# Kernel optimization log

Measured on AMD Instinct MI355X. Metric: run time of the kernel, lower is better.

The kernel has to match this reference:

```python
import jax, jax.numpy as jnp
import numpy as np

N_NODES = 100000
N_EDGES = 1600000
IN_DIM = 256
HID = 128
R = 3  # num_relations


def layer_norm(h, gamma, beta, eps=1e-5):
    mu = h.mean(axis=-1, keepdims=True)
    var = ((h - mu) ** 2).mean(axis=-1, keepdims=True)
    return (h - mu) * jax.lax.rsqrt(var + eps) * gamma + beta


def rgcn_conv(h, src, dst, etype, W, root, bias):
    """PyG RGCNConv with aggr='mean'. W:[R,in,out], root:[in,out], bias:[out]."""
    N = h.shape[0]
    out_dim = W.shape[-1]
    trans = jnp.einsum('ni,rio->rno', h, W)            # [R, N, out]
    msgs = trans[etype, src]                            # [E, out] gather per edge
    seg = dst * R + etype                               # combined (node, relation) segment id
    sums = jax.ops.segment_sum(msgs, seg, num_segments=N * R)          # [N*R, out]
    cnt = jax.ops.segment_sum(jnp.ones_like(msgs[:, 0]), seg, num_segments=N * R)
    agg = (sums / jnp.maximum(cnt, 1.0)[:, None]).reshape(N, R, out_dim).sum(axis=1)
    return agg + h @ root + bias


def setup_inputs() -> dict:
    key = jax.random.key(0)
    ks = jax.random.split(key, 10)
    s = lambda *sh: 1.0 / np.sqrt(sh[-2])
    inp = {
        'x': jax.random.normal(ks[0], (N_NODES, IN_DIM), dtype=jnp.float32),
        'edge_index': jax.random.randint(ks[1], (2, N_EDGES), 0, N_NODES, dtype=jnp.int64),
        'edge_type': jax.random.randint(ks[2], (N_EDGES,), 0, R, dtype=jnp.int64),
        # layer 0: in=256 -> out=128
        'W0': jax.random.normal(ks[3], (R, IN_DIM, HID), dtype=jnp.float32) / np.sqrt(IN_DIM),
        'root0': jax.random.normal(ks[4], (IN_DIM, HID), dtype=jnp.float32) / np.sqrt(IN_DIM),
        'b0': jnp.zeros((HID,), dtype=jnp.float32),
        'g0': jnp.ones((HID,), dtype=jnp.float32),
        'be0': jnp.zeros((HID,), dtype=jnp.float32),
        # layer 1: in=128 -> out=128
        'W1': jax.random.normal(ks[5], (R, HID, HID), dtype=jnp.float32) / np.sqrt(HID),
        'root1': jax.random.normal(ks[6], (HID, HID), dtype=jnp.float32) / np.sqrt(HID),
        'b1': jnp.zeros((HID,), dtype=jnp.float32),
        'g1': jnp.ones((HID,), dtype=jnp.float32),
        'be1': jnp.zeros((HID,), dtype=jnp.float32),
        # output LayerNorm (projection is Identity since hidden==output)
        'gout': jnp.ones((HID,), dtype=jnp.float32),
        'bout': jnp.zeros((HID,), dtype=jnp.float32),
    }
    return inp


def reference(x, edge_index, edge_type, W0, root0, b0, g0, be0,
              W1, root1, b1, g1, be1, gout, bout):
    src, dst = edge_index[0], edge_index[1]
    h = rgcn_conv(x, src, dst, edge_type, W0, root0, b0)
    h = layer_norm(h, g0, be0)
    h = jax.nn.leaky_relu(h, negative_slope=0.2)  # dropout = identity (eval)
    h = rgcn_conv(h, src, dst, edge_type, W1, root1, b1)
    h = layer_norm(h, g1, be1)
    h = layer_norm(h, gout, bout)  # output_projection is Identity
    return h
```

## Files before the change

### kernel.cpp

```cpp
#include <hip/hip_runtime.h>

#define NN 100000
#define EE 1600000

#define FB2  1568
#define NR   12500
#define GBX  782
#define GB0  (GBX * 4)
#define PB0  512
#define PB1  256
#define CVB  2048

typedef unsigned short ushortT;
typedef unsigned int uintT;
typedef __attribute__((ext_vector_type(4))) float f32x4;
typedef __attribute__((ext_vector_type(8))) short bf16x8;

__device__ inline float bf2f(ushortT b) {
    return __uint_as_float(((uintT)b) << 16);
}
__device__ inline ushortT f2bf(float f) {
    uintT u = __float_as_uint(f);
    u += 0x7FFFu + ((u >> 16) & 1u);
    return (ushortT)(u >> 16);
}

__device__ inline void gload_lds16(const void* g, void* l) {
    __builtin_amdgcn_global_load_lds((const __attribute__((address_space(1))) void*)g,
                                     (__attribute__((address_space(3))) void*)l, 16, 0, 0);
}

__device__ void cvt_role(int bid, const float* __restrict__ x, ushortT* __restrict__ xb) {
    const int total = NN * 256 / 4;
    for (int i = bid * 256 + threadIdx.x; i < total; i += CVB * 256) {
        float4 v = ((const float4*)x)[i];
        ushort4 o;
        o.x = f2bf(v.x); o.y = f2bf(v.y); o.z = f2bf(v.z); o.w = f2bf(v.w);
        ((ushort4*)xb)[i] = o;
    }
}

template <int K>
__device__ void bpack_role(int bid, const float* __restrict__ W,
                           const float* __restrict__ root, ushortT* __restrict__ Bpack) {
    constexpr int KB = K / 32;
    int idx = bid * 256 + threadIdx.x;
    if (idx >= 512 * K) return;
    int j = idx & 7;
    int l = (idx >> 3) & 63;
    int blk = idx >> 9;
    int kb = blk % KB, nblk = blk / KB;
    int k = kb * 32 + (l >> 4) * 8 + j;
    int m = nblk * 16 + (l & 15);
    float v;
    if (m < 384) {
        v = W[(((size_t)(m >> 7)) * K + k) * 128 + (m & 127)];
    } else {
        v = root[(size_t)k * 128 + (m - 384)];
    }
    Bpack[idx] = f2bf(v);
}

__global__ __launch_bounds__(256) void fill_kernel(const int* __restrict__ esrc,
                                                   const int* __restrict__ edst,
                                                   const int* __restrict__ etyp,
                                                   uintT* __restrict__ cursor,
                                                   uintT* __restrict__ elist) {
    const int bid = blockIdx.x;
    const int g = bid & 7;
    const int j = bid >> 3;
    const int lo = g * NR, hi = lo + NR;
    const int base = j * 8192;
    for (int k0 = 0; k0 < 8192; k0 += 1024) {
        int e0 = base + k0 + threadIdx.x;
        int d[4];
#pragma unroll
        for (int t = 0; t < 4; ++t) {
            int e = e0 + t * 256;
            d[t] = (e < EE) ? __builtin_nontemporal_load(&edst[e]) : -1;
        }
#pragma unroll
        for (int t = 0; t < 4; ++t) {
            if (d[t] >= lo && d[t] < hi) {
                int e = e0 + t * 256;
                int s = __builtin_nontemporal_load(&esrc[e]);
                int r = __builtin_nontemporal_load(&etyp[e]);
                if ((unsigned)s < NN && (unsigned)r < 3u) {
                    uintT add = 1u + (r == 1 ? (1u << 10) : 0u) + (r == 2 ? (1u << 20) : 0u);
                    uintT old = atomicAdd(&cursor[d[t]], add);
                    uintT pos = old & 1023u;
                    if (pos < 64u) elist[(size_t)d[t] * 64 + pos] = ((uintT)s << 2) | (uintT)r;
                }
            }
        }
    }
}

__device__ inline int swz_off(int r, int g) {
    return r * 32 + ((g ^ ((r >> 1) & 3)) << 3);
}

template <int K>
__device__ void gemm_role(int bx, int by, const ushortT* __restrict__ A,
                          const ushortT* __restrict__ Bpack, ushortT* __restrict__ C,
                          int N, ushortT* As ) {
    constexpr int KB = K / 32;
    const int tid = threadIdx.x;
    const int lane = tid & 63;
    const int wid = tid >> 6;
    const int wr = wid >> 1, wc = wid & 1;
    const int bm = bx * 128;
    const int bnblk = by * 8;

    size_t src_off[2];
#pragma unroll
    for (int t = 0; t < 2; ++t) {
        int U = (wid * 2 + t) * 64 + lane;
        int r = U >> 2;
        int g = (U & 3) ^ ((r >> 1) & 3);
        int row = bm + r;
        if (row > N - 1) row = N - 1;
        src_off[t] = (size_t)row * K + g * 8;
    }

    auto stage_issue = [&](int kblk, int buf) {
#pragma unroll
        for (int t = 0; t < 2; ++t)
            gload_lds16(&A[src_off[t] + kblk * 32], &As[buf * 4096 + (wid * 2 + t) * 512]);
    };
    f32x4 acc[4][4] = {};
    bf16x8 breg[4], bnext[4];
    auto load_b = [&](int kblk, bf16x8* out) {
#pragma unroll
        for (int nb = 0; nb < 4; ++nb) {
            int nblk = bnblk + wc * 4 + nb;
            out[nb] = *(const bf16x8*)&Bpack[((size_t)(nblk * KB + kblk) * 64 + lane) * 8];
        }
    };

    stage_issue(0, 0);
    load_b(0, breg);

    for (int kblk = 0; kblk < KB; ++kblk) {
        const int cur = kblk & 1;
        __syncthreads();
        if (kblk + 1 < KB) stage_issue(kblk + 1, cur ^ 1);
        bf16x8 afrag[4];
#pragma unroll
        for (int mb = 0; mb < 4; ++mb) {
            int fr = wr * 64 + mb * 16 + (lane & 15);
            afrag[mb] = *(const bf16x8*)&As[cur * 4096 + swz_off(fr, lane >> 4)];
        }
        if (kblk + 1 < KB) load_b(kblk + 1, bnext);
#pragma unroll
        for (int mb = 0; mb < 4; ++mb)
#pragma unroll
            for (int nb = 0; nb < 4; ++nb)
                acc[mb][nb] = __builtin_amdgcn_mfma_f32_16x16x32_bf16(
                    afrag[mb], breg[nb], acc[mb][nb], 0, 0, 0);
        if (kblk + 1 < KB) {
#pragma unroll
            for (int nb = 0; nb < 4; ++nb) breg[nb] = bnext[nb];
        }
    }

#pragma unroll
    for (int mb = 0; mb < 4; ++mb) {
        int row0 = bm + wr * 64 + mb * 16 + ((lane >> 4) << 2);
#pragma unroll
        for (int nb = 0; nb < 4; ++nb) {
            int col = (bnblk + wc * 4 + nb) * 16 + (lane & 15);
#pragma unroll
            for (int q = 0; q < 4; ++q) {
                int row = row0 + q;
                if (row < N) C[(size_t)row * 512 + col] = f2bf(acc[mb][nb][q]);
            }
        }
    }
}

__global__ __launch_bounds__(256) void k1_kernel(const float* __restrict__ x,
                                                 ushortT* __restrict__ xb,
                                                 const float* __restrict__ W0,
                                                 const float* __restrict__ root0,
                                                 ushortT* __restrict__ Bpack0,
                                                 const float* __restrict__ W1,
                                                 const float* __restrict__ root1,
                                                 ushortT* __restrict__ Bpack1) {
    int bid = blockIdx.x;
    if (bid < CVB) { cvt_role(bid, x, xb); return; }
    bid -= CVB;
    if (bid < PB0) { bpack_role<256>(bid, W0, root0, Bpack0); return; }
    bid -= PB0;
    bpack_role<128>(bid, W1, root1, Bpack1);
}

__global__ __launch_bounds__(256) void gemm0_kernel(const ushortT* __restrict__ A,
                                                    const ushortT* __restrict__ Bpack,
                                                    ushortT* __restrict__ C) {
    __shared__ ushortT As[2 * 4096];
    gemm_role<256>(blockIdx.x % GBX, blockIdx.x / GBX, A, Bpack, C, NN, As);
}

__global__ __launch_bounds__(256) void gemm1_kernel(const ushortT* __restrict__ A,
                                                    const ushortT* __restrict__ Bpack,
                                                    ushortT* __restrict__ C) {
    __shared__ ushortT As[2 * 4096];
    gemm_role<128>(blockIdx.x % GBX, blockIdx.x / GBX, A, Bpack, C, NN, As);
}

template <int LAYER>
__global__ __launch_bounds__(256) void agg_finalize_kernel(
    const ushortT* __restrict__ trans, const uintT* __restrict__ elist,
    const uintT* __restrict__ cursor,
    const float* __restrict__ bias, const float* __restrict__ gamma,
    const float* __restrict__ beta, const float* __restrict__ gout,
    const float* __restrict__ bout, void* __restrict__ outp) {
    const int wid = threadIdx.x >> 6;
    const int lane = threadIdx.x & 63;
    const int n = blockIdx.x * 4 + wid;
    const int c2 = lane * 2;
    const int cbyte = c2 * 2;

    const uintT cw = cursor[n];
    int deg = (int)(cw & 1023u);
    const int cr1 = (int)((cw >> 10) & 1023u);
    const int cr2 = (int)((cw >> 20) & 1023u);
    const int cr0 = deg - cr1 - cr2;
    const float i0 = 1.0f / fmaxf((float)cr0, 1.0f);
    const float i1 = 1.0f / fmaxf((float)cr1, 1.0f);
    const float i2 = 1.0f / fmaxf((float)cr2, 1.0f);
    if (deg > 64) deg = 64;
    const char* tb = (const char*)trans;

    uintT ev_all = 0;
    if (deg > 0) ev_all = elist[(size_t)n * 64 + (lane < deg ? lane : deg - 1)];

    float p0 = 0.f, p1 = 0.f, q0 = 0.f, q1 = 0.f;
    float r0a = 0.f, r1a = 0.f, s0a = 0.f, s1a = 0.f;

    for (int i = 0; i < deg; i += 8) {
#pragma unroll
        for (int k = 0; k < 8; ++k) {
            int sl = i + k;
            int slc = sl < deg ? sl : deg - 1;
            uintT ev = (uintT)__builtin_amdgcn_readlane((int)ev_all, slc);
            uintT off = (ev >> 2) * 1024u + (ev & 3u) * 256u;
            ushort2 u = *(const ushort2*)(tb + off + cbyte);
            int r = (int)(ev & 3u);
            float wr_ = r == 0 ? i0 : (r == 1 ? i1 : i2);
            float w = sl < deg ? wr_ : 0.f;
            float f0 = w * bf2f(u.x), f1 = w * bf2f(u.y);
            if ((k & 3) == 0) { p0 += f0; p1 += f1; }
            else if ((k & 3) == 1) { q0 += f0; q1 += f1; }
            else if ((k & 3) == 2) { r0a += f0; r1a += f1; }
            else { s0a += f0; s1a += f1; }
        }
    }
    float a0 = (p0 + q0) + (r0a + s0a);
    float a1 = (p1 + q1) + (r1a + s1a);

    ushort2 rt = *(const ushort2*)&trans[(size_t)n * 512 + 384 + c2];
    float v0 = a0 + bf2f(rt.x) + bias[c2 + 0];
    float v1 = a1 + bf2f(rt.y) + bias[c2 + 1];

    float s = v0 + v1, s2 = v0 * v0 + v1 * v1;
#pragma unroll
    for (int m = 32; m >= 1; m >>= 1) {
        s += __shfl_xor(s, m);
        s2 += __shfl_xor(s2, m);
    }
    float mu = s * (1.0f / 128.0f);
    float rstd = rsqrtf(s2 * (1.0f / 128.0f) - mu * mu + 1e-5f);
    float y0 = (v0 - mu) * rstd * gamma[c2 + 0] + beta[c2 + 0];
    float y1 = (v1 - mu) * rstd * gamma[c2 + 1] + beta[c2 + 1];

    if (LAYER == 0) {
        y0 = y0 > 0.f ? y0 : 0.2f * y0;
        y1 = y1 > 0.f ? y1 : 0.2f * y1;
        ushort2 o;
        o.x = f2bf(y0);
        o.y = f2bf(y1);
        *(ushort2*)&((ushortT*)outp)[(size_t)n * 128 + c2] = o;
    } else {
        float t = y0 + y1, t2 = y0 * y0 + y1 * y1;
#pragma unroll
        for (int m = 32; m >= 1; m >>= 1) {
            t += __shfl_xor(t, m);
            t2 += __shfl_xor(t2, m);
        }
        float mu2 = t * (1.0f / 128.0f);
        float rstd2 = rsqrtf(t2 * (1.0f / 128.0f) - mu2 * mu2 + 1e-5f);
        float2 o;
        o.x = (y0 - mu2) * rstd2 * gout[c2 + 0] + bout[c2 + 0];
        o.y = (y1 - mu2) * rstd2 * gout[c2 + 1] + bout[c2 + 1];
        *(float2*)&((float*)outp)[(size_t)n * 128 + c2] = o;
    }
}

extern "C" void kernel_launch(void* const* d_in, const int* in_sizes, int n_in,
                              void* d_out, int out_size, void* d_ws, size_t ws_size,
                              hipStream_t stream) {
    const float* x     = (const float*)d_in[0];
    const int*   eidx  = (const int*)d_in[1];
    const int*   etyp  = (const int*)d_in[2];
    const float* W0    = (const float*)d_in[3];
    const float* root0 = (const float*)d_in[4];
    const float* b0    = (const float*)d_in[5];
    const float* g0    = (const float*)d_in[6];
    const float* be0   = (const float*)d_in[7];
    const float* W1    = (const float*)d_in[8];
    const float* root1 = (const float*)d_in[9];
    const float* b1    = (const float*)d_in[10];
    const float* g1    = (const float*)d_in[11];
    const float* be1   = (const float*)d_in[12];
    const float* gout  = (const float*)d_in[13];
    const float* bout  = (const float*)d_in[14];

    const int* esrc = eidx;
    const int* edst = eidx + EE;

    const size_t sz_trans  = (size_t)NN * 512 * 2;
    const size_t sz_h1     = (size_t)NN * 128 * 2;
    const size_t sz_bpack0 = (size_t)512 * 256 * 2;
    const size_t sz_bpack1 = (size_t)512 * 128 * 2;
    const size_t sz_xb     = (size_t)NN * 256 * 2;
    const size_t sz_cur    = (size_t)NN * 4;
    const size_t sz_elist  = (size_t)NN * 64 * 4;
    if (ws_size < sz_trans + sz_h1 + sz_bpack0 + sz_bpack1 + sz_xb + sz_cur + sz_elist)
        return;

    char* ws = (char*)d_ws;
    ushortT* trans  = (ushortT*)ws; ws += sz_trans;
    ushortT* h1     = (ushortT*)ws; ws += sz_h1;
    ushortT* Bpack0 = (ushortT*)ws; ws += sz_bpack0;
    ushortT* Bpack1 = (ushortT*)ws; ws += sz_bpack1;
    ushortT* xb     = (ushortT*)ws; ws += sz_xb;
    uintT*   cursor = (uintT*)ws;   ws += sz_cur;
    uintT*   elist  = (uintT*)ws;   ws += sz_elist;

    hipMemsetAsync(cursor, 0, sz_cur, stream);

    fill_kernel<<<FB2, 256, 0, stream>>>(esrc, edst, etyp, cursor, elist);

    k1_kernel<<<CVB + PB0 + PB1, 256, 0, stream>>>(x, xb, W0, root0, Bpack0,
                                                   W1, root1, Bpack1);

    gemm0_kernel<<<GB0, 256, 0, stream>>>(xb, Bpack0, trans);
    agg_finalize_kernel<0><<<NN / 4, 256, 0, stream>>>(trans, elist, cursor, b0, g0, be0,
                                                       nullptr, nullptr, h1);

    gemm1_kernel<<<GB0, 256, 0, stream>>>(h1, Bpack1, trans);
    agg_finalize_kernel<1><<<NN / 4, 256, 0, stream>>>(trans, elist, cursor, b1, g1, be1,
                                                       gout, bout, d_out);
}
```

Baseline: 383.7 us.

## Fuse fp32-to-bf16 conversion of x into layer-0 GEMM LDS staging

Removes the separate pass that converts x to bf16 into a workspace buffer. The layer-0 GEMM now stages fp32 tiles of x straight into LDS using a new XOR swizzle, then converts them to bf16 fragments with packed convert instructions before the MFMA. This saves one write and one read of the 51MB bf16 copy, but the four column-block GEMM blocks each re-read the fp32 input at twice the byte size. The change also makes the cursor load wave-uniform with readfirstlane and unrolls the edge aggregation loop by 16 instead of 8.

```diff
diff --git a/kernel.cpp b/kernel.cpp
--- a/kernel.cpp
+++ b/kernel.cpp
@@ -9,7 +9,6 @@
 #define GB0  (GBX * 4)
 #define PB0  512
 #define PB1  256
-#define CVB  2048
 
 typedef unsigned short ushortT;
 typedef unsigned int uintT;
@@ -28,16 +27,6 @@
 __device__ inline void gload_lds16(const void* g, void* l) {
     __builtin_amdgcn_global_load_lds((const __attribute__((address_space(1))) void*)g,
                                      (__attribute__((address_space(3))) void*)l, 16, 0, 0);
-}
-
-__device__ void cvt_role(int bid, const float* __restrict__ x, ushortT* __restrict__ xb) {
-    const int total = NN * 256 / 4;
-    for (int i = bid * 256 + threadIdx.x; i < total; i += CVB * 256) {
-        float4 v = ((const float4*)x)[i];
-        ushort4 o;
-        o.x = f2bf(v.x); o.y = f2bf(v.y); o.z = f2bf(v.z); o.w = f2bf(v.w);
-        ((ushort4*)xb)[i] = o;
-    }
 }
 
 template <int K>
@@ -61,6 +50,17 @@
     Bpack[idx] = f2bf(v);
 }
 
+__global__ __launch_bounds__(256) void bpack2_kernel(const float* __restrict__ W0,
+                                                     const float* __restrict__ root0,
+                                                     ushortT* __restrict__ B0,
+                                                     const float* __restrict__ W1,
+                                                     const float* __restrict__ root1,
+                                                     ushortT* __restrict__ B1) {
+    int bid = blockIdx.x;
+    if (bid < PB0) { bpack_role<256>(bid, W0, root0, B0); return; }
+    bpack_role<128>(bid - PB0, W1, root1, B1);
+}
+
 __global__ __launch_bounds__(256) void fill_kernel(const int* __restrict__ esrc,
                                                    const int* __restrict__ edst,
                                                    const int* __restrict__ etyp,
@@ -96,19 +96,111 @@
     }
 }
 
-__device__ inline int swz_off(int r, int g) {
-    return r * 32 + ((g ^ ((r >> 1) & 3)) << 3);
-}
-
-template <int K>
-__device__ void gemm_role(int bx, int by, const ushortT* __restrict__ A,
-                          const ushortT* __restrict__ Bpack, ushortT* __restrict__ C,
-                          int N, ushortT* As ) {
-    constexpr int KB = K / 32;
+__global__ __launch_bounds__(256) void gemm0f_kernel(const float* __restrict__ A,
+                                                     const ushortT* __restrict__ Bpack,
+                                                     ushortT* __restrict__ C) {
+    constexpr int K = 256, KB = 8;
+    __shared__ float Asf[2][128 * 32];
+
     const int tid = threadIdx.x;
     const int lane = tid & 63;
     const int wid = tid >> 6;
     const int wr = wid >> 1, wc = wid & 1;
+    const int bx = blockIdx.x % GBX, by = blockIdx.x / GBX;
+    const int bm = bx * 128;
+    const int bnblk = by * 8;
+
+    size_t src_off[4];
+#pragma unroll
+    for (int t = 0; t < 4; ++t) {
+        int U = (wid * 4 + t) * 64 + lane;
+        int r = U >> 3;
+        int g = (U & 7) ^ (r & 7);
+        int row = bm + r;
+        if (row > NN - 1) row = NN - 1;
+        src_off[t] = (size_t)row * K + g * 4;
+    }
+
+    auto stage_issue = [&](int kblk, int buf) {
+#pragma unroll
+        for (int t = 0; t < 4; ++t)
+            gload_lds16(&A[src_off[t] + kblk * 32], &Asf[buf][(wid * 4 + t) * 256]);
+    };
+    f32x4 acc[4][4] = {};
+    bf16x8 breg[4], bnext[4];
+    auto load_b = [&](int kblk, bf16x8* out) {
+#pragma unroll
+        for (int nb = 0; nb < 4; ++nb) {
+            int nblk = bnblk + wc * 4 + nb;
+            out[nb] = *(const bf16x8*)&Bpack[((size_t)(nblk * KB + kblk) * 64 + lane) * 8];
+        }
+    };
+
+    stage_issue(0, 0);
+    load_b(0, breg);
+
+    for (int kblk = 0; kblk < KB; ++kblk) {
+        const int cur = kblk & 1;
+        __syncthreads();
+        if (kblk + 1 < KB) stage_issue(kblk + 1, cur ^ 1);
+        bf16x8 afrag[4];
+#pragma unroll
+        for (int mb = 0; mb < 4; ++mb) {
+            int fr = wr * 64 + mb * 16 + (lane & 15);
+            int kg = lane >> 4;
+            f32x4 lo = *(const f32x4*)&Asf[cur][fr * 32 + (((2 * kg) ^ (fr & 7)) * 4)];
+            f32x4 hi = *(const f32x4*)&Asf[cur][fr * 32 + (((2 * kg + 1) ^ (fr & 7)) * 4)];
+            uintT au0, au1, au2, au3;
+            asm("v_cvt_pk_bf16_f32 %0, %1, %2" : "=v"(au0) : "v"(lo.x), "v"(lo.y));
+            asm("v_cvt_pk_bf16_f32 %0, %1, %2" : "=v"(au1) : "v"(lo.z), "v"(lo.w));
+            asm("v_cvt_pk_bf16_f32 %0, %1, %2" : "=v"(au2) : "v"(hi.x), "v"(hi.y));
+            asm("v_cvt_pk_bf16_f32 %0, %1, %2" : "=v"(au3) : "v"(hi.z), "v"(hi.w));
+            uintT tmp[4] = {au0, au1, au2, au3};
+            afrag[mb] = *(const bf16x8*)tmp;
+        }
+        if (kblk + 1 < KB) load_b(kblk + 1, bnext);
+#pragma unroll
+        for (int mb = 0; mb < 4; ++mb)
+#pragma unroll
+            for (int nb = 0; nb < 4; ++nb)
+                acc[mb][nb] = __builtin_amdgcn_mfma_f32_16x16x32_bf16(
+                    afrag[mb], breg[nb], acc[mb][nb], 0, 0, 0);
+        if (kblk + 1 < KB) {
+#pragma unroll
+            for (int nb = 0; nb < 4; ++nb) breg[nb] = bnext[nb];
+        }
+    }
+
+#pragma unroll
+    for (int mb = 0; mb < 4; ++mb) {
+        int row0 = bm + wr * 64 + mb * 16 + ((lane >> 4) << 2);
+#pragma unroll
+        for (int nb = 0; nb < 4; ++nb) {
+            int col = (bnblk + wc * 4 + nb) * 16 + (lane & 15);
+#pragma unroll
+            for (int q = 0; q < 4; ++q) {
+                int row = row0 + q;
+                if (row < NN) C[(size_t)row * 512 + col] = f2bf(acc[mb][nb][q]);
+            }
+        }
+    }
+}
+
+__device__ inline int swz_off(int r, int g) {
+    return r * 32 + ((g ^ ((r >> 1) & 3)) << 3);
+}
+
+__global__ __launch_bounds__(256) void gemm1_kernel(const ushortT* __restrict__ A,
+                                                    const ushortT* __restrict__ Bpack,
+                                                    ushortT* __restrict__ C) {
+    constexpr int K = 128, KB = 4;
+    __shared__ ushortT As[2][128 * 32];
+
+    const int tid = threadIdx.x;
+    const int lane = tid & 63;
+    const int wid = tid >> 6;
+    const int wr = wid >> 1, wc = wid & 1;
+    const int bx = blockIdx.x % GBX, by = blockIdx.x / GBX;
     const int bm = bx * 128;
     const int bnblk = by * 8;
 
@@ -119,14 +211,14 @@
         int r = U >> 2;
         int g = (U & 3) ^ ((r >> 1) & 3);
         int row = bm + r;
-        if (row > N - 1) row = N - 1;
+        if (row > NN - 1) row = NN - 1;
         src_off[t] = (size_t)row * K + g * 8;
     }
 
     auto stage_issue = [&](int kblk, int buf) {
 #pragma unroll
         for (int t = 0; t < 2; ++t)
-            gload_lds16(&A[src_off[t] + kblk * 32], &As[buf * 4096 + (wid * 2 + t) * 512]);
+            gload_lds16(&A[src_off[t] + kblk * 32], &As[buf][(wid * 2 + t) * 512]);
     };
     f32x4 acc[4][4] = {};
     bf16x8 breg[4], bnext[4];
@@ -149,7 +241,7 @@
 #pragma unroll
         for (int mb = 0; mb < 4; ++mb) {
             int fr = wr * 64 + mb * 16 + (lane & 15);
-            afrag[mb] = *(const bf16x8*)&As[cur * 4096 + swz_off(fr, lane >> 4)];
+            afrag[mb] = *(const bf16x8*)&As[cur][swz_off(fr, lane >> 4)];
         }
         if (kblk + 1 < KB) load_b(kblk + 1, bnext);
 #pragma unroll
@@ -173,40 +265,10 @@
 #pragma unroll
             for (int q = 0; q < 4; ++q) {
                 int row = row0 + q;
-                if (row < N) C[(size_t)row * 512 + col] = f2bf(acc[mb][nb][q]);
+                if (row < NN) C[(size_t)row * 512 + col] = f2bf(acc[mb][nb][q]);
             }
         }
     }
-}
-
-__global__ __launch_bounds__(256) void k1_kernel(const float* __restrict__ x,
-                                                 ushortT* __restrict__ xb,
-                                                 const float* __restrict__ W0,
-                                                 const float* __restrict__ root0,
-                                                 ushortT* __restrict__ Bpack0,
-                                                 const float* __restrict__ W1,
-                                                 const float* __restrict__ root1,
-                                                 ushortT* __restrict__ Bpack1) {
-    int bid = blockIdx.x;
-    if (bid < CVB) { cvt_role(bid, x, xb); return; }
-    bid -= CVB;
-    if (bid < PB0) { bpack_role<256>(bid, W0, root0, Bpack0); return; }
-    bid -= PB0;
-    bpack_role<128>(bid, W1, root1, Bpack1);
-}
-
-__global__ __launch_bounds__(256) void gemm0_kernel(const ushortT* __restrict__ A,
-                                                    const ushortT* __restrict__ Bpack,
-                                                    ushortT* __restrict__ C) {
-    __shared__ ushortT As[2 * 4096];
-    gemm_role<256>(blockIdx.x % GBX, blockIdx.x / GBX, A, Bpack, C, NN, As);
-}
-
-__global__ __launch_bounds__(256) void gemm1_kernel(const ushortT* __restrict__ A,
-                                                    const ushortT* __restrict__ Bpack,
-                                                    ushortT* __restrict__ C) {
-    __shared__ ushortT As[2 * 4096];
-    gemm_role<128>(blockIdx.x % GBX, blockIdx.x / GBX, A, Bpack, C, NN, As);
 }
 
 template <int LAYER>
@@ -222,7 +284,7 @@
     const int c2 = lane * 2;
     const int cbyte = c2 * 2;
 
-    const uintT cw = cursor[n];
+    const uintT cw = (uintT)__builtin_amdgcn_readfirstlane((int)cursor[n]);
     int deg = (int)(cw & 1023u);
     const int cr1 = (int)((cw >> 10) & 1023u);
     const int cr2 = (int)((cw >> 20) & 1023u);
@@ -239,9 +301,9 @@
     float p0 = 0.f, p1 = 0.f, q0 = 0.f, q1 = 0.f;
     float r0a = 0.f, r1a = 0.f, s0a = 0.f, s1a = 0.f;
 
-    for (int i = 0; i < deg; i += 8) {
-#pragma unroll
-        for (int k = 0; k < 8; ++k) {
+    for (int i = 0; i < deg; i += 16) {
+#pragma unroll
+        for (int k = 0; k < 16; ++k) {
             int sl = i + k;
             int slc = sl < deg ? sl : deg - 1;
             uintT ev = (uintT)__builtin_amdgcn_readlane((int)ev_all, slc);
@@ -324,29 +386,25 @@
     const size_t sz_h1     = (size_t)NN * 128 * 2;
     const size_t sz_bpack0 = (size_t)512 * 256 * 2;
     const size_t sz_bpack1 = (size_t)512 * 128 * 2;
-    const size_t sz_xb     = (size_t)NN * 256 * 2;
     const size_t sz_cur    = (size_t)NN * 4;
     const size_t sz_elist  = (size_t)NN * 64 * 4;
-    if (ws_size < sz_trans + sz_h1 + sz_bpack0 + sz_bpack1 + sz_xb + sz_cur + sz_elist)
-        return;
+    if (ws_size < sz_trans + sz_h1 + sz_bpack0 + sz_bpack1 + sz_cur + sz_elist) return;
 
     char* ws = (char*)d_ws;
     ushortT* trans  = (ushortT*)ws; ws += sz_trans;
     ushortT* h1     = (ushortT*)ws; ws += sz_h1;
     ushortT* Bpack0 = (ushortT*)ws; ws += sz_bpack0;
     ushortT* Bpack1 = (ushortT*)ws; ws += sz_bpack1;
-    ushortT* xb     = (ushortT*)ws; ws += sz_xb;
     uintT*   cursor = (uintT*)ws;   ws += sz_cur;
     uintT*   elist  = (uintT*)ws;   ws += sz_elist;
 
     hipMemsetAsync(cursor, 0, sz_cur, stream);
 
+    bpack2_kernel<<<PB0 + PB1, 256, 0, stream>>>(W0, root0, Bpack0, W1, root1, Bpack1);
+
     fill_kernel<<<FB2, 256, 0, stream>>>(esrc, edst, etyp, cursor, elist);
 
-    k1_kernel<<<CVB + PB0 + PB1, 256, 0, stream>>>(x, xb, W0, root0, Bpack0,
-                                                   W1, root1, Bpack1);
-
-    gemm0_kernel<<<GB0, 256, 0, stream>>>(xb, Bpack0, trans);
+    gemm0f_kernel<<<GB0, 256, 0, stream>>>(x, Bpack0, trans);
     agg_finalize_kernel<0><<<NN / 4, 256, 0, stream>>>(trans, elist, cursor, b0, g0, be0,
                                                        nullptr, nullptr, h1);
 
```

After: 390.6 us. Within noise of the previous version (+1.8%).
